# Kernel tuning notes

Measured on AMD Instinct MI355X. Metric: run time of the kernel, lower is better.

The kernel has to match this reference:

```python
import jax, jax.numpy as jnp
import numpy as np

N = 50000      # nodes
E = 800000     # edges
G = 512        # graphs
H = 256        # hidden_dim
T = 32         # tag embedding dim
L = 4          # num_layers
EPS = 1e-5


def setup_inputs() -> dict:
    key = jax.random.key(0)
    ks = jax.random.split(key, 16)
    x = jax.random.randint(ks[0], (N,), 0, 100)
    tags = jax.random.randint(ks[1], (N,), 0, 3)
    edge_index = jax.random.randint(ks[2], (2, E), 0, N)
    batch = jnp.sort(jax.random.randint(ks[3], (N,), 0, G))
    s = 1.0 / np.sqrt(H)
    atom_emb = jax.random.normal(ks[4], (100, H), jnp.float32)
    tag_emb = jax.random.normal(ks[5], (3, T), jnp.float32)
    Wp = jax.random.normal(ks[6], (H + T, H), jnp.float32) * (1.0 / np.sqrt(H + T))
    bp = jnp.zeros((H,), jnp.float32)
    gcn_W = jax.random.normal(ks[7], (L, H, H), jnp.float32) * s
    gcn_b = jnp.zeros((L, H), jnp.float32)
    bn_g = jnp.ones((L, H), jnp.float32)
    bn_b = jnp.zeros((L, H), jnp.float32)
    W1 = jax.random.normal(ks[8], (H, H // 2), jnp.float32) * s
    b1 = jnp.zeros((H // 2,), jnp.float32)
    W2 = jax.random.normal(ks[9], (H // 2, 1), jnp.float32) * (1.0 / np.sqrt(H // 2))
    b2 = jnp.zeros((1,), jnp.float32)
    return dict(x=x, tags=tags, edge_index=edge_index, batch=batch,
                atom_emb=atom_emb, tag_emb=tag_emb, Wp=Wp, bp=bp,
                gcn_W=gcn_W, gcn_b=gcn_b, bn_g=bn_g, bn_b=bn_b,
                W1=W1, b1=b1, W2=W2, b2=b2)


def _gcn_conv(h, W, b, src, dst, dinv):
    # PyG GCNConv: x' = W x, symmetric normalization with self-loops.
    hw = h @ W                                   # [N, H]
    norm = dinv[src] * dinv[dst]                 # [E]
    msg = hw[src] * norm[:, None]                # [E, H]  (gather)
    agg = jax.ops.segment_sum(msg, dst, num_segments=N)  # scatter-add
    agg = agg + hw * (dinv * dinv)[:, None]      # self-loop term
    return agg + b


def _batch_norm(x, g, b):
    mu = jnp.mean(x, axis=0)
    var = jnp.var(x, axis=0)
    return (x - mu) * jax.lax.rsqrt(var + EPS) * g + b


def reference(x, tags, edge_index, batch, atom_emb, tag_emb, Wp, bp,
              gcn_W, gcn_b, bn_g, bn_b, W1, b1, W2, b2):
    src, dst = edge_index[0], edge_index[1]
    # degree with self-loops (gcn_norm counts on the dst/col index)
    deg = jax.ops.segment_sum(jnp.ones((E,), jnp.float32), dst, num_segments=N) + 1.0
    dinv = jax.lax.rsqrt(deg)

    h = jnp.concatenate([atom_emb[x], tag_emb[tags]], axis=1) @ Wp + bp  # [N, H]
    for l in range(L):
        res = h
        h = _gcn_conv(h, gcn_W[l], gcn_b[l], src, dst, dinv)
        h = jax.nn.relu(_batch_norm(h, bn_g[l], bn_b[l]))
        h = h + res                                  # dropout is identity in eval

    # global mean pool over graphs
    sums = jax.ops.segment_sum(h, batch, num_segments=G)
    cnts = jax.ops.segment_sum(jnp.ones((N,), jnp.float32), batch, num_segments=G)
    pooled = sums / jnp.maximum(cnts, 1.0)[:, None]  # [G, H]

    hid = jax.nn.relu(pooled @ W1 + b1)
    energy = hid @ W2 + b2                           # [G, 1]
    return energy.squeeze(-1)
```

## Files before the change

kernel.cpp:

```cpp
#include <hip/hip_runtime.h>
#include <hip/hip_bf16.h>

#define NN 50000
#define EE 800000
#define GG 512
#define HH 256
#define TT 32
#define LL 4
#define EPSF 1e-5f

typedef __attribute__((ext_vector_type(8))) short short8;
typedef __attribute__((ext_vector_type(4))) float float4v;

__device__ inline unsigned short f2b(float f) {
    unsigned u = __float_as_uint(f);
    unsigned r = (u + 0x7FFFu + ((u >> 16) & 1u)) >> 16;
    return (unsigned short)r;
}
__device__ inline float4 bf4_to_f4(ushort4 u) {
    float4 f;
    f.x = __uint_as_float((unsigned)u.x << 16);
    f.y = __uint_as_float((unsigned)u.y << 16);
    f.z = __uint_as_float((unsigned)u.z << 16);
    f.w = __uint_as_float((unsigned)u.w << 16);
    return f;
}

__global__ void k_degree(const int* __restrict__ dst, int* __restrict__ cnt, int E) {
    int e = blockIdx.x * 256 + threadIdx.x;
    if (e < E) atomicAdd(&cnt[dst[e]], 1);
}

__global__ void k_dinv(const int* __restrict__ cnt, float* __restrict__ dinv, int N) {
    int i = blockIdx.x * 256 + threadIdx.x;
    if (i < N) dinv[i] = rsqrtf((float)cnt[i] + 1.0f);
}

__global__ void k_scan1(const int* __restrict__ cnt, int* __restrict__ incl,
                        int* __restrict__ bsum, int N) {
    __shared__ int s[1024];
    int i = blockIdx.x * 1024 + threadIdx.x;
    int v = (i < N) ? cnt[i] : 0;
    s[threadIdx.x] = v;
    __syncthreads();
    for (int off = 1; off < 1024; off <<= 1) {
        int t = (threadIdx.x >= off) ? s[threadIdx.x - off] : 0;
        __syncthreads();
        s[threadIdx.x] += t;
        __syncthreads();
    }
    if (i < N) incl[i] = s[threadIdx.x];
    if (threadIdx.x == 1023) bsum[blockIdx.x] = s[1023];
}

__global__ void k_scan2(int* __restrict__ bsum, int nb) {
    __shared__ int s[64];
    int v = (threadIdx.x < nb) ? bsum[threadIdx.x] : 0;
    s[threadIdx.x] = v;
    __syncthreads();
    for (int off = 1; off < 64; off <<= 1) {
        int t = (threadIdx.x >= off) ? s[threadIdx.x - off] : 0;
        __syncthreads();
        s[threadIdx.x] += t;
        __syncthreads();
    }
    if (threadIdx.x < nb) bsum[threadIdx.x] = s[threadIdx.x] - v;
}

__global__ void k_scan3(int* __restrict__ rs, const int* __restrict__ cnt,
                        const int* __restrict__ boff, int N) {
    int i = blockIdx.x * 256 + threadIdx.x;
    if (i < N) rs[i] = rs[i] + boff[i >> 10] - cnt[i];
}

__global__ void k_scatter(const int* __restrict__ src, const int* __restrict__ dst,
                          const int* __restrict__ rs, int* __restrict__ cur,
                          int* __restrict__ csr, int E) {
    int e = blockIdx.x * 256 + threadIdx.x;
    if (e >= E) return;
    int d = dst[e];
    int p = rs[d] + atomicAdd(&cur[d], 1);
    csr[p] = src[e];
}

__global__ void k_wprep(const float* __restrict__ W, unsigned short* __restrict__ Wt) {
    int l = blockIdx.y;
    int n = blockIdx.x * 4 + (threadIdx.x >> 6);
    int kq = (threadIdx.x & 63) * 4;
    const float* Wl = W + (size_t)l * HH * HH;
    ushort4 o;
    o.x = f2b(Wl[(size_t)(kq + 0) * HH + n]);
    o.y = f2b(Wl[(size_t)(kq + 1) * HH + n]);
    o.z = f2b(Wl[(size_t)(kq + 2) * HH + n]);
    o.w = f2b(Wl[(size_t)(kq + 3) * HH + n]);
    *(ushort4*)(Wt + (size_t)l * HH * HH + (size_t)n * HH + kq) = o;
}

__global__ void k_proj(const float* __restrict__ atom_emb, const float* __restrict__ tag_emb,
                       const float* __restrict__ Wp, const float* __restrict__ bp,
                       float* __restrict__ aref, float* __restrict__ tref) {
    int r = blockIdx.x;
    int j = threadIdx.x;
    if (r < 100) {
        float acc = bp[j];
        for (int k = 0; k < HH; ++k) acc += atom_emb[r * HH + k] * Wp[(size_t)k * HH + j];
        aref[r * HH + j] = acc;
    } else {
        int tr = r - 100;
        float acc = 0.f;
        for (int k = 0; k < TT; ++k) acc += tag_emb[tr * TT + k] * Wp[(size_t)(HH + k) * HH + j];
        tref[tr * HH + j] = acc;
    }
}

__global__ void k_h0(const int* __restrict__ x, const int* __restrict__ tags,
                     const float* __restrict__ aref, const float* __restrict__ tref,
                     unsigned short* __restrict__ hb, int N) {
    int n = blockIdx.x;
    int lane = threadIdx.x;
    float4 a = ((const float4*)(aref + (size_t)x[n] * HH))[lane];
    float4 t = ((const float4*)(tref + (size_t)tags[n] * HH))[lane];
    ushort4 u;
    u.x = f2b(a.x + t.x); u.y = f2b(a.y + t.y);
    u.z = f2b(a.z + t.z); u.w = f2b(a.w + t.w);
    ((ushort4*)(hb + (size_t)n * HH))[lane] = u;
}

__global__ __launch_bounds__(256) void k_gemm(const unsigned short* __restrict__ hb,
                                              const unsigned short* __restrict__ Wt,
                                              const float* __restrict__ dinv,
                                              unsigned short* __restrict__ hwb, int M) {
    __shared__ unsigned short As[128][72];
    __shared__ unsigned short Bs[128][72];
    int t = threadIdx.x;
    int lane = t & 63, w = t >> 6;
    int wr = w >> 1, wc = w & 1;
    int l15 = lane & 15, l4 = lane >> 4;
    int row0 = blockIdx.y * 128, col0 = blockIdx.x * 128;
    float4v acc[4][4];
#pragma unroll
    for (int i = 0; i < 4; ++i)
#pragma unroll
        for (int j = 0; j < 4; ++j) acc[i][j] = (float4v)0.f;

    for (int k0 = 0; k0 < 256; k0 += 64) {
        if (k0) __syncthreads();
#pragma unroll
        for (int u = 0; u < 4; ++u) {
            int idx = u * 256 + t;
            int r = idx >> 3;
            int c = (idx & 7) * 8;
            *(uint4*)&As[r][c] = *(const uint4*)(hb + (size_t)(row0 + r) * 256 + k0 + c);
            *(uint4*)&Bs[r][c] = *(const uint4*)(Wt + (size_t)(col0 + r) * 256 + k0 + c);
        }
        __syncthreads();
#pragma unroll
        for (int kk = 0; kk < 64; kk += 32) {
            short8 a[4], b[4];
#pragma unroll
            for (int i = 0; i < 4; ++i)
                a[i] = *(const short8*)&As[wr * 64 + i * 16 + l15][kk + l4 * 8];
#pragma unroll
            for (int i = 0; i < 4; ++i)
                b[i] = *(const short8*)&Bs[wc * 64 + i * 16 + l15][kk + l4 * 8];
#pragma unroll
            for (int mi = 0; mi < 4; ++mi)
#pragma unroll
                for (int ni = 0; ni < 4; ++ni)
                    acc[mi][ni] = __builtin_amdgcn_mfma_f32_16x16x32_bf16(
                        a[mi], b[ni], acc[mi][ni], 0, 0, 0);
        }
    }
#pragma unroll
    for (int mi = 0; mi < 4; ++mi) {
        int mb = row0 + wr * 64 + mi * 16 + l4 * 4;
        float dv[4];
#pragma unroll
        for (int r = 0; r < 4; ++r) dv[r] = (mb + r < M) ? dinv[mb + r] : 0.f;
#pragma unroll
        for (int ni = 0; ni < 4; ++ni) {
            int n = col0 + wc * 64 + ni * 16 + l15;
#pragma unroll
            for (int r = 0; r < 4; ++r) {
                if (mb + r < M)
                    hwb[(size_t)(mb + r) * 256 + n] = f2b(acc[mi][ni][r] * dv[r]);
            }
        }
    }
}

__global__ void k_agg(const unsigned short* __restrict__ hwb, float* __restrict__ agg,
                      const int* __restrict__ csr, const int* __restrict__ rs,
                      const int* __restrict__ cnt, const float* __restrict__ dinv,
                      const float* __restrict__ bias, int N) {
    int wave = threadIdx.x >> 6;
    int lane = threadIdx.x & 63;
    int n = blockIdx.x * 4 + wave;
    if (n >= N) return;
    float dn = dinv[n];
    int e = rs[n];
    int end = e + cnt[n];
    float4 acc = bf4_to_f4(((const ushort4*)(hwb + (size_t)n * HH))[lane]);
    for (; e + 8 <= end; e += 8) {
        int s0 = csr[e],     s1 = csr[e + 1], s2 = csr[e + 2], s3 = csr[e + 3];
        int s4 = csr[e + 4], s5 = csr[e + 5], s6 = csr[e + 6], s7 = csr[e + 7];
        float4 m0 = bf4_to_f4(((const ushort4*)(hwb + (size_t)s0 * HH))[lane]);
        float4 m1 = bf4_to_f4(((const ushort4*)(hwb + (size_t)s1 * HH))[lane]);
        float4 m2 = bf4_to_f4(((const ushort4*)(hwb + (size_t)s2 * HH))[lane]);
        float4 m3 = bf4_to_f4(((const ushort4*)(hwb + (size_t)s3 * HH))[lane]);
        float4 m4 = bf4_to_f4(((const ushort4*)(hwb + (size_t)s4 * HH))[lane]);
        float4 m5 = bf4_to_f4(((const ushort4*)(hwb + (size_t)s5 * HH))[lane]);
        float4 m6 = bf4_to_f4(((const ushort4*)(hwb + (size_t)s6 * HH))[lane]);
        float4 m7 = bf4_to_f4(((const ushort4*)(hwb + (size_t)s7 * HH))[lane]);
        acc.x += ((m0.x + m1.x) + (m2.x + m3.x)) + ((m4.x + m5.x) + (m6.x + m7.x));
        acc.y += ((m0.y + m1.y) + (m2.y + m3.y)) + ((m4.y + m5.y) + (m6.y + m7.y));
        acc.z += ((m0.z + m1.z) + (m2.z + m3.z)) + ((m4.z + m5.z) + (m6.z + m7.z));
        acc.w += ((m0.w + m1.w) + (m2.w + m3.w)) + ((m4.w + m5.w) + (m6.w + m7.w));
    }
    for (; e + 4 <= end; e += 4) {
        int s0 = csr[e], s1 = csr[e + 1], s2 = csr[e + 2], s3 = csr[e + 3];
        float4 m0 = bf4_to_f4(((const ushort4*)(hwb + (size_t)s0 * HH))[lane]);
        float4 m1 = bf4_to_f4(((const ushort4*)(hwb + (size_t)s1 * HH))[lane]);
        float4 m2 = bf4_to_f4(((const ushort4*)(hwb + (size_t)s2 * HH))[lane]);
        float4 m3 = bf4_to_f4(((const ushort4*)(hwb + (size_t)s3 * HH))[lane]);
        acc.x += (m0.x + m1.x) + (m2.x + m3.x);
        acc.y += (m0.y + m1.y) + (m2.y + m3.y);
        acc.z += (m0.z + m1.z) + (m2.z + m3.z);
        acc.w += (m0.w + m1.w) + (m2.w + m3.w);
    }
    for (; e < end; ++e) {
        int s = csr[e];
        float4 m = bf4_to_f4(((const ushort4*)(hwb + (size_t)s * HH))[lane]);
        acc.x += m.x; acc.y += m.y; acc.z += m.z; acc.w += m.w;
    }
    float4 b = ((const float4*)bias)[lane];
    float4 r;
    r.x = acc.x * dn + b.x; r.y = acc.y * dn + b.y;
    r.z = acc.z * dn + b.z; r.w = acc.w * dn + b.w;
    ((float4*)(agg + (size_t)n * HH))[lane] = r;
}

__global__ __launch_bounds__(256) void k_bnstats(const float4* __restrict__ agg,
                                                 float* __restrict__ colsum,
                                                 float* __restrict__ colsq, int N) {
    __shared__ float4 ssum[4][64];
    __shared__ float4 ssq[4][64];
    int lane = threadIdx.x & 63;
    int wv = threadIdx.x >> 6;
    int rows_per = (N + gridDim.x - 1) / gridDim.x;
    int r0 = blockIdx.x * rows_per;
    int r1 = r0 + rows_per; if (r1 > N) r1 = N;
    float4 s = make_float4(0.f, 0.f, 0.f, 0.f);
    float4 s2 = make_float4(0.f, 0.f, 0.f, 0.f);
    for (int r = r0 + wv; r < r1; r += 4) {
        float4 v = agg[(size_t)r * 64 + lane];
        s.x += v.x; s.y += v.y; s.z += v.z; s.w += v.w;
        s2.x += v.x * v.x; s2.y += v.y * v.y; s2.z += v.z * v.z; s2.w += v.w * v.w;
    }
    ssum[wv][lane] = s;
    ssq[wv][lane] = s2;
    __syncthreads();
    int j = lane * 4;
    if (wv == 0) {
        float4 a = ssum[0][lane], b = ssum[1][lane], c = ssum[2][lane], d = ssum[3][lane];
        atomicAdd(&colsum[j + 0], a.x + b.x + c.x + d.x);
        atomicAdd(&colsum[j + 1], a.y + b.y + c.y + d.y);
        atomicAdd(&colsum[j + 2], a.z + b.z + c.z + d.z);
        atomicAdd(&colsum[j + 3], a.w + b.w + c.w + d.w);
    } else if (wv == 1) {
        float4 a = ssq[0][lane], b = ssq[1][lane], c = ssq[2][lane], d = ssq[3][lane];
        atomicAdd(&colsq[j + 0], a.x + b.x + c.x + d.x);
        atomicAdd(&colsq[j + 1], a.y + b.y + c.y + d.y);
        atomicAdd(&colsq[j + 2], a.z + b.z + c.z + d.z);
        atomicAdd(&colsq[j + 3], a.w + b.w + c.w + d.w);
    }
}

__global__ void k_epi(const float4* __restrict__ agg, ushort4* __restrict__ hb,
                      const float4* __restrict__ colsum, const float4* __restrict__ colsq,
                      const float4* __restrict__ g4, const float4* __restrict__ b4,
                      int total, float invN) {
    int idx = blockIdx.x * 256 + threadIdx.x;
    if (idx >= total) return;
    int q = idx & 63;
    float4 a = agg[idx];
    float4 s = colsum[q], s2 = colsq[q], g = g4[q], b = b4[q];
    float4 hv = bf4_to_f4(hb[idx]);
    float mu, var, v;
    mu = s.x * invN; var = s2.x * invN - mu * mu;
    v = (a.x - mu) * rsqrtf(var + EPSF) * g.x + b.x; hv.x += fmaxf(v, 0.f);
    mu = s.y * invN; var = s2.y * invN - mu * mu;
    v = (a.y - mu) * rsqrtf(var + EPSF) * g.y + b.y; hv.y += fmaxf(v, 0.f);
    mu = s.z * invN; var = s2.z * invN - mu * mu;
    v = (a.z - mu) * rsqrtf(var + EPSF) * g.z + b.z; hv.z += fmaxf(v, 0.f);
    mu = s.w * invN; var = s2.w * invN - mu * mu;
    v = (a.w - mu) * rsqrtf(var + EPSF) * g.w + b.w; hv.w += fmaxf(v, 0.f);
    ushort4 u;
    u.x = f2b(hv.x); u.y = f2b(hv.y); u.z = f2b(hv.z); u.w = f2b(hv.w);
    hb[idx] = u;
}

__global__ void k_ginit(int* __restrict__ gstart, int G, int N) {
    int g = blockIdx.x * 256 + threadIdx.x;
    if (g <= G) gstart[g] = N;
}

__global__ void k_gbound(const int* __restrict__ batch, int* __restrict__ gstart, int N) {
    int n = blockIdx.x * 256 + threadIdx.x;
    if (n >= N) return;
    int b = batch[n];
    int prev = (n == 0) ? -1 : batch[n - 1];
    for (int g = prev + 1; g <= b; ++g) gstart[g] = n;
}

__global__ void k_pool(const unsigned short* __restrict__ hb, const int* __restrict__ gstart,
                       float* __restrict__ pooled) {
    __shared__ float4 sm[4][64];
    int g = blockIdx.x;
    int t = threadIdx.x;
    int lane = t & 63, wv = t >> 6;
    int s = gstart[g], e = gstart[g + 1];
    float4 acc = make_float4(0.f, 0.f, 0.f, 0.f);
    for (int n = s + wv; n < e; n += 4) {
        float4 v = bf4_to_f4(((const ushort4*)(hb + (size_t)n * HH))[lane]);
        acc.x += v.x; acc.y += v.y; acc.z += v.z; acc.w += v.w;
    }
    sm[wv][lane] = acc;
    __syncthreads();
    if (wv == 0) {
        float4 a = sm[0][lane], b = sm[1][lane], c = sm[2][lane], d = sm[3][lane];
        float inv = 1.0f / fmaxf((float)(e - s), 1.0f);
        float4 r;
        r.x = (a.x + b.x + c.x + d.x) * inv;
        r.y = (a.y + b.y + c.y + d.y) * inv;
        r.z = (a.z + b.z + c.z + d.z) * inv;
        r.w = (a.w + b.w + c.w + d.w) * inv;
        ((float4*)pooled)[(size_t)g * 64 + lane] = r;
    }
}

__global__ void k_head(const float* __restrict__ pooled,
                       const float* __restrict__ W1, const float* __restrict__ b1,
                       const float* __restrict__ W2, const float* __restrict__ b2,
                       float* __restrict__ out) {
    __shared__ float prow[256];
    __shared__ float hred[128];
    int g = blockIdx.x, t = threadIdx.x;
    prow[t] = pooled[(size_t)g * HH + t];
    prow[t + 128] = pooled[(size_t)g * HH + t + 128];
    __syncthreads();
    float acc = b1[t];
    for (int k = 0; k < HH; ++k) acc += prow[k] * W1[(size_t)k * 128 + t];
    float hid = fmaxf(acc, 0.f);
    hred[t] = hid * W2[t];
    __syncthreads();
    for (int off = 64; off > 0; off >>= 1) {
        if (t < off) hred[t] += hred[t + off];
        __syncthreads();
    }
    if (t == 0) out[g] = hred[0] + b2[0];
}

extern "C" void kernel_launch(void* const* d_in, const int* in_sizes, int n_in,
                              void* d_out, int out_size, void* d_ws, size_t ws_size,
                              hipStream_t stream) {
    const int* x        = (const int*)d_in[0];
    const int* tags     = (const int*)d_in[1];
    const int* ei       = (const int*)d_in[2];
    const int* batch    = (const int*)d_in[3];
    const float* atom_e = (const float*)d_in[4];
    const float* tag_e  = (const float*)d_in[5];
    const float* Wp     = (const float*)d_in[6];
    const float* bp     = (const float*)d_in[7];
    const float* gcn_W  = (const float*)d_in[8];
    const float* gcn_b  = (const float*)d_in[9];
    const float* bn_g   = (const float*)d_in[10];
    const float* bn_b   = (const float*)d_in[11];
    const float* W1     = (const float*)d_in[12];
    const float* b1     = (const float*)d_in[13];
    const float* W2     = (const float*)d_in[14];
    const float* b2     = (const float*)d_in[15];
    float* out = (float*)d_out;

    const int N = NN, E = EE, G = GG, H = HH;
    const int Mpad = ((N + 127) / 128) * 128;

    char* p = (char*)d_ws;
    auto alloc = [&](size_t bytes) {
        void* r = (void*)p;
        p += (bytes + 255) & ~(size_t)255;
        return r;
    };
    unsigned short* hb  = (unsigned short*)alloc((size_t)Mpad * H * 2);
    unsigned short* hwb = (unsigned short*)alloc((size_t)Mpad * H * 2);
    unsigned short* Wt  = (unsigned short*)alloc((size_t)LL * H * H * 2);
    float* agg  = (float*)alloc((size_t)N * H * 4);
    float* dinv = (float*)alloc((size_t)N * 4);
    int* cnt    = (int*)alloc((size_t)N * 4);
    int* rs     = (int*)alloc((size_t)N * 4);
    int* cur    = (int*)alloc((size_t)N * 4);
    int* csr    = (int*)alloc((size_t)E * 4);
    int* bsum   = (int*)alloc(64 * 4);
    float* aref = (float*)alloc(100 * (size_t)H * 4);
    float* tref = (float*)alloc(3 * (size_t)H * 4);
    float* cstat= (float*)alloc(2 * (size_t)H * 4);
    int* gstart = (int*)alloc((size_t)(G + 1) * 4);
    float* pooled = (float*)alloc((size_t)G * H * 4);

    const int* src = ei;
    const int* dst = ei + E;

    hipMemsetAsync(cnt, 0, (size_t)N * 4, stream);
    hipMemsetAsync(cur, 0, (size_t)N * 4, stream);

    k_degree<<<(E + 255) / 256, 256, 0, stream>>>(dst, cnt, E);
    k_dinv<<<(N + 255) / 256, 256, 0, stream>>>(cnt, dinv, N);

    int nb = (N + 1023) / 1024;
    k_scan1<<<nb, 1024, 0, stream>>>(cnt, rs, bsum, N);
    k_scan2<<<1, 64, 0, stream>>>(bsum, nb);
    k_scan3<<<(N + 255) / 256, 256, 0, stream>>>(rs, cnt, bsum, N);
    k_scatter<<<(E + 255) / 256, 256, 0, stream>>>(src, dst, rs, cur, csr, E);

    k_ginit<<<(G + 256) / 256, 256, 0, stream>>>(gstart, G, N);
    k_gbound<<<(N + 255) / 256, 256, 0, stream>>>(batch, gstart, N);

    k_wprep<<<dim3(64, LL), 256, 0, stream>>>(gcn_W, Wt);
    k_proj<<<103, 256, 0, stream>>>(atom_e, tag_e, Wp, bp, aref, tref);
    k_h0<<<N, 64, 0, stream>>>(x, tags, aref, tref, hb, N);

    for (int l = 0; l < LL; ++l) {
        k_gemm<<<dim3(2, Mpad / 128), 256, 0, stream>>>(
            hb, Wt + (size_t)l * H * H, dinv, hwb, N);
        k_agg<<<(N + 3) / 4, 256, 0, stream>>>(hwb, agg, csr, rs, cnt, dinv,
                                               gcn_b + (size_t)l * H, N);
        hipMemsetAsync(cstat, 0, 2 * (size_t)H * 4, stream);
        k_bnstats<<<512, 256, 0, stream>>>((const float4*)agg, cstat, cstat + H, N);
        k_epi<<<(N * 64 + 255) / 256, 256, 0, stream>>>(
            (const float4*)agg, (ushort4*)hb,
            (const float4*)cstat, (const float4*)(cstat + H),
            (const float4*)(bn_g + (size_t)l * H), (const float4*)(bn_b + (size_t)l * H),
            N * 64, 1.0f / (float)N);
    }

    k_pool<<<G, 256, 0, stream>>>(hb, gstart, pooled);
    k_head<<<G, 128, 0, stream>>>(pooled, W1, b1, W2, b2, out);
}
```

Baseline: 899.9 us.

## Fuse whole GNN pipeline into one cooperative persistent megakernel

Replaces the chain of many small kernel launches (degree, scan, CSR build, projection, per-layer GEMM/aggregate/batchnorm/epilogue, pooling, head) with a single cooperative kernel using grid-wide syncs between phases. The aggregate buffer is stored in bf16 instead of fp32, and the final layer's batchnorm/residual epilogue is folded into the pooling pass. This targets launch overhead and reduces memory traffic, at the cost of grid-sync latency and possibly lower occupancy for the GEMM and gather phases.

```diff
diff --git a/kernel.cpp b/kernel.cpp
--- a/kernel.cpp
+++ b/kernel.cpp
@@ -1,5 +1,8 @@
 #include <hip/hip_runtime.h>
 #include <hip/hip_bf16.h>
+#include <hip/hip_cooperative_groups.h>
+
+namespace cg = cooperative_groups;
 
 #define NN 50000
 #define EE 800000
@@ -8,6 +11,7 @@
 #define TT 32
 #define LL 4
 #define EPSF 1e-5f
+#define MPAD 50048
 
 typedef __attribute__((ext_vector_type(8))) short short8;
 typedef __attribute__((ext_vector_type(4))) float float4v;
@@ -16,6 +20,10 @@
     unsigned u = __float_as_uint(f);
     unsigned r = (u + 0x7FFFu + ((u >> 16) & 1u)) >> 16;
     return (unsigned short)r;
+}
+__device__ inline unsigned pack2(float lo, float hi) {
+    __hip_bfloat162 b2 = __float22bfloat162_rn(float2{lo, hi});
+    return *reinterpret_cast<unsigned*>(&b2);
 }
 __device__ inline float4 bf4_to_f4(ushort4 u) {
     float4 f;
@@ -26,339 +34,388 @@
     return f;
 }
 
-__global__ void k_degree(const int* __restrict__ dst, int* __restrict__ cnt, int E) {
-    int e = blockIdx.x * 256 + threadIdx.x;
-    if (e < E) atomicAdd(&cnt[dst[e]], 1);
-}
-
-__global__ void k_dinv(const int* __restrict__ cnt, float* __restrict__ dinv, int N) {
-    int i = blockIdx.x * 256 + threadIdx.x;
-    if (i < N) dinv[i] = rsqrtf((float)cnt[i] + 1.0f);
-}
-
-__global__ void k_scan1(const int* __restrict__ cnt, int* __restrict__ incl,
-                        int* __restrict__ bsum, int N) {
-    __shared__ int s[1024];
-    int i = blockIdx.x * 1024 + threadIdx.x;
-    int v = (i < N) ? cnt[i] : 0;
-    s[threadIdx.x] = v;
-    __syncthreads();
-    for (int off = 1; off < 1024; off <<= 1) {
-        int t = (threadIdx.x >= off) ? s[threadIdx.x - off] : 0;
+__global__ __launch_bounds__(256, 4) void k_mega(
+    const int* __restrict__ x, const int* __restrict__ tags,
+    const int* __restrict__ ei, const int* __restrict__ batch,
+    const float* __restrict__ atom_e, const float* __restrict__ tag_e,
+    const float* __restrict__ Wp, const float* __restrict__ bp,
+    const float* __restrict__ gcn_W, const float* __restrict__ gcn_b,
+    const float* __restrict__ bn_g, const float* __restrict__ bn_b,
+    const float* __restrict__ W1, const float* __restrict__ b1,
+    const float* __restrict__ W2, const float* __restrict__ b2,
+    float* __restrict__ out,
+    unsigned short* __restrict__ hb, unsigned short* __restrict__ hwb,
+    unsigned short* __restrict__ Wt, unsigned short* __restrict__ aggb,
+    float* __restrict__ dinv, int* __restrict__ rs, int* __restrict__ csr,
+    int* __restrict__ bsum, float* __restrict__ aref, float* __restrict__ tref,
+    int* __restrict__ gstart, float* __restrict__ pooled,
+    int* __restrict__ cnt, int* __restrict__ cur, float* __restrict__ cstat) {
+
+    cg::grid_group gg = cg::this_grid();
+    __shared__ __align__(16) char smem[36864];
+
+    const int* src = ei;
+    const int* dst = ei + EE;
+    const int T = blockIdx.x * 256 + threadIdx.x;
+    const int NT = gridDim.x * 256;
+    const float invN = 1.0f / (float)NN;
+
+    for (int e = T; e < EE; e += NT) atomicAdd(&cnt[dst[e]], 1);
+    gg.sync();
+
+    const int nch = (NN + 255) / 256;
+    {
+        int* si = (int*)smem;
+        for (int ch = blockIdx.x; ch < nch; ch += gridDim.x) {
+            int i = ch * 256 + threadIdx.x;
+            int v = (i < NN) ? cnt[i] : 0;
+            si[threadIdx.x] = v;
+            __syncthreads();
+            for (int off = 1; off < 256; off <<= 1) {
+                int t = (threadIdx.x >= off) ? si[threadIdx.x - off] : 0;
+                __syncthreads();
+                si[threadIdx.x] += t;
+                __syncthreads();
+            }
+            if (i < NN) rs[i] = si[threadIdx.x];
+            if (threadIdx.x == 255) bsum[ch] = si[255];
+            __syncthreads();
+        }
+    }
+    gg.sync();
+
+    if (blockIdx.x == 0) {
+        int* si = (int*)smem;
+        int v = (threadIdx.x < nch) ? bsum[threadIdx.x] : 0;
+        si[threadIdx.x] = v;
         __syncthreads();
-        s[threadIdx.x] += t;
-        __syncthreads();
-    }
-    if (i < N) incl[i] = s[threadIdx.x];
-    if (threadIdx.x == 1023) bsum[blockIdx.x] = s[1023];
-}
-
-__global__ void k_scan2(int* __restrict__ bsum, int nb) {
-    __shared__ int s[64];
-    int v = (threadIdx.x < nb) ? bsum[threadIdx.x] : 0;
-    s[threadIdx.x] = v;
-    __syncthreads();
-    for (int off = 1; off < 64; off <<= 1) {
-        int t = (threadIdx.x >= off) ? s[threadIdx.x - off] : 0;
-        __syncthreads();
-        s[threadIdx.x] += t;
-        __syncthreads();
-    }
-    if (threadIdx.x < nb) bsum[threadIdx.x] = s[threadIdx.x] - v;
-}
-
-__global__ void k_scan3(int* __restrict__ rs, const int* __restrict__ cnt,
-                        const int* __restrict__ boff, int N) {
-    int i = blockIdx.x * 256 + threadIdx.x;
-    if (i < N) rs[i] = rs[i] + boff[i >> 10] - cnt[i];
-}
-
-__global__ void k_scatter(const int* __restrict__ src, const int* __restrict__ dst,
-                          const int* __restrict__ rs, int* __restrict__ cur,
-                          int* __restrict__ csr, int E) {
-    int e = blockIdx.x * 256 + threadIdx.x;
-    if (e >= E) return;
-    int d = dst[e];
-    int p = rs[d] + atomicAdd(&cur[d], 1);
-    csr[p] = src[e];
-}
-
-__global__ void k_wprep(const float* __restrict__ W, unsigned short* __restrict__ Wt) {
-    int l = blockIdx.y;
-    int n = blockIdx.x * 4 + (threadIdx.x >> 6);
-    int kq = (threadIdx.x & 63) * 4;
-    const float* Wl = W + (size_t)l * HH * HH;
-    ushort4 o;
-    o.x = f2b(Wl[(size_t)(kq + 0) * HH + n]);
-    o.y = f2b(Wl[(size_t)(kq + 1) * HH + n]);
-    o.z = f2b(Wl[(size_t)(kq + 2) * HH + n]);
-    o.w = f2b(Wl[(size_t)(kq + 3) * HH + n]);
-    *(ushort4*)(Wt + (size_t)l * HH * HH + (size_t)n * HH + kq) = o;
-}
-
-__global__ void k_proj(const float* __restrict__ atom_emb, const float* __restrict__ tag_emb,
-                       const float* __restrict__ Wp, const float* __restrict__ bp,
-                       float* __restrict__ aref, float* __restrict__ tref) {
-    int r = blockIdx.x;
-    int j = threadIdx.x;
-    if (r < 100) {
-        float acc = bp[j];
-        for (int k = 0; k < HH; ++k) acc += atom_emb[r * HH + k] * Wp[(size_t)k * HH + j];
-        aref[r * HH + j] = acc;
-    } else {
-        int tr = r - 100;
-        float acc = 0.f;
-        for (int k = 0; k < TT; ++k) acc += tag_emb[tr * TT + k] * Wp[(size_t)(HH + k) * HH + j];
-        tref[tr * HH + j] = acc;
-    }
-}
-
-__global__ void k_h0(const int* __restrict__ x, const int* __restrict__ tags,
-                     const float* __restrict__ aref, const float* __restrict__ tref,
-                     unsigned short* __restrict__ hb, int N) {
-    int n = blockIdx.x;
-    int lane = threadIdx.x;
-    float4 a = ((const float4*)(aref + (size_t)x[n] * HH))[lane];
-    float4 t = ((const float4*)(tref + (size_t)tags[n] * HH))[lane];
-    ushort4 u;
-    u.x = f2b(a.x + t.x); u.y = f2b(a.y + t.y);
-    u.z = f2b(a.z + t.z); u.w = f2b(a.w + t.w);
-    ((ushort4*)(hb + (size_t)n * HH))[lane] = u;
-}
-
-__global__ __launch_bounds__(256) void k_gemm(const unsigned short* __restrict__ hb,
-                                              const unsigned short* __restrict__ Wt,
-                                              const float* __restrict__ dinv,
-                                              unsigned short* __restrict__ hwb, int M) {
-    __shared__ unsigned short As[128][72];
-    __shared__ unsigned short Bs[128][72];
-    int t = threadIdx.x;
-    int lane = t & 63, w = t >> 6;
-    int wr = w >> 1, wc = w & 1;
-    int l15 = lane & 15, l4 = lane >> 4;
-    int row0 = blockIdx.y * 128, col0 = blockIdx.x * 128;
-    float4v acc[4][4];
-#pragma unroll
-    for (int i = 0; i < 4; ++i)
-#pragma unroll
-        for (int j = 0; j < 4; ++j) acc[i][j] = (float4v)0.f;
-
-    for (int k0 = 0; k0 < 256; k0 += 64) {
-        if (k0) __syncthreads();
-#pragma unroll
-        for (int u = 0; u < 4; ++u) {
-            int idx = u * 256 + t;
-            int r = idx >> 3;
-            int c = (idx & 7) * 8;
-            *(uint4*)&As[r][c] = *(const uint4*)(hb + (size_t)(row0 + r) * 256 + k0 + c);
-            *(uint4*)&Bs[r][c] = *(const uint4*)(Wt + (size_t)(col0 + r) * 256 + k0 + c);
-        }
-        __syncthreads();
-#pragma unroll
-        for (int kk = 0; kk < 64; kk += 32) {
-            short8 a[4], b[4];
-#pragma unroll
-            for (int i = 0; i < 4; ++i)
-                a[i] = *(const short8*)&As[wr * 64 + i * 16 + l15][kk + l4 * 8];
-#pragma unroll
-            for (int i = 0; i < 4; ++i)
-                b[i] = *(const short8*)&Bs[wc * 64 + i * 16 + l15][kk + l4 * 8];
-#pragma unroll
-            for (int mi = 0; mi < 4; ++mi)
-#pragma unroll
-                for (int ni = 0; ni < 4; ++ni)
-                    acc[mi][ni] = __builtin_amdgcn_mfma_f32_16x16x32_bf16(
-                        a[mi], b[ni], acc[mi][ni], 0, 0, 0);
-        }
-    }
-#pragma unroll
-    for (int mi = 0; mi < 4; ++mi) {
-        int mb = row0 + wr * 64 + mi * 16 + l4 * 4;
-        float dv[4];
-#pragma unroll
-        for (int r = 0; r < 4; ++r) dv[r] = (mb + r < M) ? dinv[mb + r] : 0.f;
-#pragma unroll
-        for (int ni = 0; ni < 4; ++ni) {
-            int n = col0 + wc * 64 + ni * 16 + l15;
-#pragma unroll
-            for (int r = 0; r < 4; ++r) {
-                if (mb + r < M)
-                    hwb[(size_t)(mb + r) * 256 + n] = f2b(acc[mi][ni][r] * dv[r]);
-            }
-        }
-    }
-}
-
-__global__ void k_agg(const unsigned short* __restrict__ hwb, float* __restrict__ agg,
-                      const int* __restrict__ csr, const int* __restrict__ rs,
-                      const int* __restrict__ cnt, const float* __restrict__ dinv,
-                      const float* __restrict__ bias, int N) {
-    int wave = threadIdx.x >> 6;
-    int lane = threadIdx.x & 63;
-    int n = blockIdx.x * 4 + wave;
-    if (n >= N) return;
-    float dn = dinv[n];
-    int e = rs[n];
-    int end = e + cnt[n];
-    float4 acc = bf4_to_f4(((const ushort4*)(hwb + (size_t)n * HH))[lane]);
-    for (; e + 8 <= end; e += 8) {
-        int s0 = csr[e],     s1 = csr[e + 1], s2 = csr[e + 2], s3 = csr[e + 3];
-        int s4 = csr[e + 4], s5 = csr[e + 5], s6 = csr[e + 6], s7 = csr[e + 7];
-        float4 m0 = bf4_to_f4(((const ushort4*)(hwb + (size_t)s0 * HH))[lane]);
-        float4 m1 = bf4_to_f4(((const ushort4*)(hwb + (size_t)s1 * HH))[lane]);
-        float4 m2 = bf4_to_f4(((const ushort4*)(hwb + (size_t)s2 * HH))[lane]);
-        float4 m3 = bf4_to_f4(((const ushort4*)(hwb + (size_t)s3 * HH))[lane]);
-        float4 m4 = bf4_to_f4(((const ushort4*)(hwb + (size_t)s4 * HH))[lane]);
-        float4 m5 = bf4_to_f4(((const ushort4*)(hwb + (size_t)s5 * HH))[lane]);
-        float4 m6 = bf4_to_f4(((const ushort4*)(hwb + (size_t)s6 * HH))[lane]);
-        float4 m7 = bf4_to_f4(((const ushort4*)(hwb + (size_t)s7 * HH))[lane]);
-        acc.x += ((m0.x + m1.x) + (m2.x + m3.x)) + ((m4.x + m5.x) + (m6.x + m7.x));
-        acc.y += ((m0.y + m1.y) + (m2.y + m3.y)) + ((m4.y + m5.y) + (m6.y + m7.y));
-        acc.z += ((m0.z + m1.z) + (m2.z + m3.z)) + ((m4.z + m5.z) + (m6.z + m7.z));
-        acc.w += ((m0.w + m1.w) + (m2.w + m3.w)) + ((m4.w + m5.w) + (m6.w + m7.w));
-    }
-    for (; e + 4 <= end; e += 4) {
-        int s0 = csr[e], s1 = csr[e + 1], s2 = csr[e + 2], s3 = csr[e + 3];
-        float4 m0 = bf4_to_f4(((const ushort4*)(hwb + (size_t)s0 * HH))[lane]);
-        float4 m1 = bf4_to_f4(((const ushort4*)(hwb + (size_t)s1 * HH))[lane]);
-        float4 m2 = bf4_to_f4(((const ushort4*)(hwb + (size_t)s2 * HH))[lane]);
-        float4 m3 = bf4_to_f4(((const ushort4*)(hwb + (size_t)s3 * HH))[lane]);
-        acc.x += (m0.x + m1.x) + (m2.x + m3.x);
-        acc.y += (m0.y + m1.y) + (m2.y + m3.y);
-        acc.z += (m0.z + m1.z) + (m2.z + m3.z);
-        acc.w += (m0.w + m1.w) + (m2.w + m3.w);
-    }
-    for (; e < end; ++e) {
-        int s = csr[e];
-        float4 m = bf4_to_f4(((const ushort4*)(hwb + (size_t)s * HH))[lane]);
-        acc.x += m.x; acc.y += m.y; acc.z += m.z; acc.w += m.w;
-    }
-    float4 b = ((const float4*)bias)[lane];
-    float4 r;
-    r.x = acc.x * dn + b.x; r.y = acc.y * dn + b.y;
-    r.z = acc.z * dn + b.z; r.w = acc.w * dn + b.w;
-    ((float4*)(agg + (size_t)n * HH))[lane] = r;
-}
-
-__global__ __launch_bounds__(256) void k_bnstats(const float4* __restrict__ agg,
-                                                 float* __restrict__ colsum,
-                                                 float* __restrict__ colsq, int N) {
-    __shared__ float4 ssum[4][64];
-    __shared__ float4 ssq[4][64];
-    int lane = threadIdx.x & 63;
-    int wv = threadIdx.x >> 6;
-    int rows_per = (N + gridDim.x - 1) / gridDim.x;
-    int r0 = blockIdx.x * rows_per;
-    int r1 = r0 + rows_per; if (r1 > N) r1 = N;
-    float4 s = make_float4(0.f, 0.f, 0.f, 0.f);
-    float4 s2 = make_float4(0.f, 0.f, 0.f, 0.f);
-    for (int r = r0 + wv; r < r1; r += 4) {
-        float4 v = agg[(size_t)r * 64 + lane];
-        s.x += v.x; s.y += v.y; s.z += v.z; s.w += v.w;
-        s2.x += v.x * v.x; s2.y += v.y * v.y; s2.z += v.z * v.z; s2.w += v.w * v.w;
-    }
-    ssum[wv][lane] = s;
-    ssq[wv][lane] = s2;
-    __syncthreads();
-    int j = lane * 4;
-    if (wv == 0) {
-        float4 a = ssum[0][lane], b = ssum[1][lane], c = ssum[2][lane], d = ssum[3][lane];
-        atomicAdd(&colsum[j + 0], a.x + b.x + c.x + d.x);
-        atomicAdd(&colsum[j + 1], a.y + b.y + c.y + d.y);
-        atomicAdd(&colsum[j + 2], a.z + b.z + c.z + d.z);
-        atomicAdd(&colsum[j + 3], a.w + b.w + c.w + d.w);
-    } else if (wv == 1) {
-        float4 a = ssq[0][lane], b = ssq[1][lane], c = ssq[2][lane], d = ssq[3][lane];
-        atomicAdd(&colsq[j + 0], a.x + b.x + c.x + d.x);
-        atomicAdd(&colsq[j + 1], a.y + b.y + c.y + d.y);
-        atomicAdd(&colsq[j + 2], a.z + b.z + c.z + d.z);
-        atomicAdd(&colsq[j + 3], a.w + b.w + c.w + d.w);
-    }
-}
-
-__global__ void k_epi(const float4* __restrict__ agg, ushort4* __restrict__ hb,
-                      const float4* __restrict__ colsum, const float4* __restrict__ colsq,
-                      const float4* __restrict__ g4, const float4* __restrict__ b4,
-                      int total, float invN) {
-    int idx = blockIdx.x * 256 + threadIdx.x;
-    if (idx >= total) return;
-    int q = idx & 63;
-    float4 a = agg[idx];
-    float4 s = colsum[q], s2 = colsq[q], g = g4[q], b = b4[q];
-    float4 hv = bf4_to_f4(hb[idx]);
-    float mu, var, v;
-    mu = s.x * invN; var = s2.x * invN - mu * mu;
-    v = (a.x - mu) * rsqrtf(var + EPSF) * g.x + b.x; hv.x += fmaxf(v, 0.f);
-    mu = s.y * invN; var = s2.y * invN - mu * mu;
-    v = (a.y - mu) * rsqrtf(var + EPSF) * g.y + b.y; hv.y += fmaxf(v, 0.f);
-    mu = s.z * invN; var = s2.z * invN - mu * mu;
-    v = (a.z - mu) * rsqrtf(var + EPSF) * g.z + b.z; hv.z += fmaxf(v, 0.f);
-    mu = s.w * invN; var = s2.w * invN - mu * mu;
-    v = (a.w - mu) * rsqrtf(var + EPSF) * g.w + b.w; hv.w += fmaxf(v, 0.f);
-    ushort4 u;
-    u.x = f2b(hv.x); u.y = f2b(hv.y); u.z = f2b(hv.z); u.w = f2b(hv.w);
-    hb[idx] = u;
-}
-
-__global__ void k_ginit(int* __restrict__ gstart, int G, int N) {
-    int g = blockIdx.x * 256 + threadIdx.x;
-    if (g <= G) gstart[g] = N;
-}
-
-__global__ void k_gbound(const int* __restrict__ batch, int* __restrict__ gstart, int N) {
-    int n = blockIdx.x * 256 + threadIdx.x;
-    if (n >= N) return;
-    int b = batch[n];
-    int prev = (n == 0) ? -1 : batch[n - 1];
-    for (int g = prev + 1; g <= b; ++g) gstart[g] = n;
-}
-
-__global__ void k_pool(const unsigned short* __restrict__ hb, const int* __restrict__ gstart,
-                       float* __restrict__ pooled) {
-    __shared__ float4 sm[4][64];
-    int g = blockIdx.x;
-    int t = threadIdx.x;
-    int lane = t & 63, wv = t >> 6;
-    int s = gstart[g], e = gstart[g + 1];
-    float4 acc = make_float4(0.f, 0.f, 0.f, 0.f);
-    for (int n = s + wv; n < e; n += 4) {
-        float4 v = bf4_to_f4(((const ushort4*)(hb + (size_t)n * HH))[lane]);
-        acc.x += v.x; acc.y += v.y; acc.z += v.z; acc.w += v.w;
-    }
-    sm[wv][lane] = acc;
-    __syncthreads();
-    if (wv == 0) {
-        float4 a = sm[0][lane], b = sm[1][lane], c = sm[2][lane], d = sm[3][lane];
-        float inv = 1.0f / fmaxf((float)(e - s), 1.0f);
-        float4 r;
-        r.x = (a.x + b.x + c.x + d.x) * inv;
-        r.y = (a.y + b.y + c.y + d.y) * inv;
-        r.z = (a.z + b.z + c.z + d.z) * inv;
-        r.w = (a.w + b.w + c.w + d.w) * inv;
-        ((float4*)pooled)[(size_t)g * 64 + lane] = r;
-    }
-}
-
-__global__ void k_head(const float* __restrict__ pooled,
-                       const float* __restrict__ W1, const float* __restrict__ b1,
-                       const float* __restrict__ W2, const float* __restrict__ b2,
-                       float* __restrict__ out) {
-    __shared__ float prow[256];
-    __shared__ float hred[128];
-    int g = blockIdx.x, t = threadIdx.x;
-    prow[t] = pooled[(size_t)g * HH + t];
-    prow[t + 128] = pooled[(size_t)g * HH + t + 128];
-    __syncthreads();
-    float acc = b1[t];
-    for (int k = 0; k < HH; ++k) acc += prow[k] * W1[(size_t)k * 128 + t];
-    float hid = fmaxf(acc, 0.f);
-    hred[t] = hid * W2[t];
-    __syncthreads();
-    for (int off = 64; off > 0; off >>= 1) {
-        if (t < off) hred[t] += hred[t + off];
-        __syncthreads();
-    }
-    if (t == 0) out[g] = hred[0] + b2[0];
+        for (int off = 1; off < 256; off <<= 1) {
+            int t = (threadIdx.x >= off) ? si[threadIdx.x - off] : 0;
+            __syncthreads();
+            si[threadIdx.x] += t;
+            __syncthreads();
+        }
+        if (threadIdx.x < nch) bsum[threadIdx.x] = si[threadIdx.x] - v;
+    }
+    gg.sync();
+
+    for (int i = T; i < NN; i += NT) {
+        int c = cnt[i];
+        rs[i] = rs[i] + bsum[i >> 8] - c;
+        dinv[i] = rsqrtf((float)c + 1.0f);
+    }
+    gg.sync();
+
+    for (int e = T; e < EE; e += NT) {
+        int d = dst[e];
+        int p = rs[d] + atomicAdd(&cur[d], 1);
+        csr[p] = src[e];
+    }
+    for (int n = T; n < NN; n += NT) {
+        int b = batch[n];
+        int prev = (n == 0) ? -1 : batch[n - 1];
+        for (int g = prev + 1; g <= b; ++g) gstart[g] = n;
+        if (n == NN - 1)
+            for (int g = b + 1; g <= GG; ++g) gstart[g] = NN;
+    }
+    for (int it = T; it < LL * 256 * 64; it += NT) {
+        int l = it >> 14;
+        int rem = it & 16383;
+        int n = rem >> 6;
+        int kq = (rem & 63) * 4;
+        const float* Wl = gcn_W + (size_t)l * HH * HH;
+        ushort4 o;
+        o.x = f2b(Wl[(size_t)(kq + 0) * HH + n]);
+        o.y = f2b(Wl[(size_t)(kq + 1) * HH + n]);
+        o.z = f2b(Wl[(size_t)(kq + 2) * HH + n]);
+        o.w = f2b(Wl[(size_t)(kq + 3) * HH + n]);
+        *(ushort4*)(Wt + (size_t)l * HH * HH + (size_t)n * HH + kq) = o;
+    }
+    for (int it = T; it < 103 * 256; it += NT) {
+        int r = it >> 8;
+        int j = it & 255;
+        if (r < 100) {
+            float acc = bp[j];
+            for (int k = 0; k < HH; ++k) acc += atom_e[r * HH + k] * Wp[(size_t)k * HH + j];
+            aref[r * HH + j] = acc;
+        } else {
+            int tr = r - 100;
+            float acc = 0.f;
+            for (int k = 0; k < TT; ++k) acc += tag_e[tr * TT + k] * Wp[(size_t)(HH + k) * HH + j];
+            tref[tr * HH + j] = acc;
+        }
+    }
+    gg.sync();
+
+    for (int i = T; i < NN * 64; i += NT) {
+        int n = i >> 6, lane = i & 63;
+        float4 a = ((const float4*)(aref + (size_t)x[n] * HH))[lane];
+        float4 t4 = ((const float4*)(tref + (size_t)tags[n] * HH))[lane];
+        unsigned lo = pack2(a.x + t4.x, a.y + t4.y);
+        unsigned hi = pack2(a.z + t4.z, a.w + t4.w);
+        ((uint2*)hb)[i] = make_uint2(lo, hi);
+    }
+    gg.sync();
+
+    for (int l = 0; l < LL; ++l) {
+        if (l > 0) {
+            float* sc = (float*)smem;
+            float* sh = sc + 256;
+            {
+                int t = threadIdx.x;
+                const float* cs = cstat + (size_t)(l - 1) * 512;
+                float mu = cs[t] * invN;
+                float var = cs[256 + t] * invN - mu * mu;
+                float s = bn_g[(size_t)(l - 1) * HH + t] * rsqrtf(var + EPSF);
+                sc[t] = s;
+                sh[t] = bn_b[(size_t)(l - 1) * HH + t] - mu * s;
+            }
+            __syncthreads();
+            for (int i = T; i < NN * 64; i += NT) {
+                int q = (i & 63) * 4;
+                float4 a = bf4_to_f4(((const ushort4*)aggb)[i]);
+                float4 hv = bf4_to_f4(((const ushort4*)hb)[i]);
+                hv.x += fmaxf(a.x * sc[q + 0] + sh[q + 0], 0.f);
+                hv.y += fmaxf(a.y * sc[q + 1] + sh[q + 1], 0.f);
+                hv.z += fmaxf(a.z * sc[q + 2] + sh[q + 2], 0.f);
+                hv.w += fmaxf(a.w * sc[q + 3] + sh[q + 3], 0.f);
+                unsigned lo = pack2(hv.x, hv.y);
+                unsigned hi = pack2(hv.z, hv.w);
+                ((uint2*)hb)[i] = make_uint2(lo, hi);
+            }
+            gg.sync();
+        }
+
+        {
+            unsigned short (*As)[72] = (unsigned short(*)[72])smem;
+            unsigned short (*Bs)[72] = (unsigned short(*)[72])(smem + 18432);
+            const unsigned short* Wl = Wt + (size_t)l * HH * HH;
+            int t = threadIdx.x;
+            int lane = t & 63, w = t >> 6;
+            int wr = w >> 1, wc = w & 1;
+            int l15 = lane & 15, l4 = lane >> 4;
+            int ntile = (MPAD / 128) * 2;
+            for (int job = blockIdx.x; job < ntile; job += gridDim.x) {
+                int row0 = (job >> 1) * 128, col0 = (job & 1) * 128;
+                float4v acc[4][4];
+#pragma unroll
+                for (int i = 0; i < 4; ++i)
+#pragma unroll
+                    for (int j = 0; j < 4; ++j) acc[i][j] = (float4v)0.f;
+                for (int k0 = 0; k0 < 256; k0 += 64) {
+                    __syncthreads();
+#pragma unroll
+                    for (int u = 0; u < 4; ++u) {
+                        int idx = u * 256 + t;
+                        int r = idx >> 3;
+                        int c = (idx & 7) * 8;
+                        int grow = row0 + r;
+                        uint4 av = make_uint4(0u, 0u, 0u, 0u);
+                        if (grow < NN) av = *(const uint4*)(hb + (size_t)grow * 256 + k0 + c);
+                        *(uint4*)&As[r][c] = av;
+                        *(uint4*)&Bs[r][c] = *(const uint4*)(Wl + (size_t)(col0 + r) * 256 + k0 + c);
+                    }
+                    __syncthreads();
+#pragma unroll
+                    for (int kk = 0; kk < 64; kk += 32) {
+                        short8 a[4], b[4];
+#pragma unroll
+                        for (int i = 0; i < 4; ++i)
+                            a[i] = *(const short8*)&As[wr * 64 + i * 16 + l15][kk + l4 * 8];
+#pragma unroll
+                        for (int i = 0; i < 4; ++i)
+                            b[i] = *(const short8*)&Bs[wc * 64 + i * 16 + l15][kk + l4 * 8];
+#pragma unroll
+                        for (int mi = 0; mi < 4; ++mi)
+#pragma unroll
+                            for (int ni = 0; ni < 4; ++ni)
+                                acc[mi][ni] = __builtin_amdgcn_mfma_f32_16x16x32_bf16(
+                                    a[mi], b[ni], acc[mi][ni], 0, 0, 0);
+                    }
+                }
+#pragma unroll
+                for (int mi = 0; mi < 4; ++mi) {
+                    int mb = row0 + wr * 64 + mi * 16 + l4 * 4;
+                    float dv[4];
+#pragma unroll
+                    for (int r = 0; r < 4; ++r) dv[r] = (mb + r < NN) ? dinv[mb + r] : 0.f;
+#pragma unroll
+                    for (int ni = 0; ni < 4; ++ni) {
+                        int n = col0 + wc * 64 + ni * 16 + l15;
+#pragma unroll
+                        for (int r = 0; r < 4; ++r) {
+                            if (mb + r < NN)
+                                hwb[(size_t)(mb + r) * 256 + n] = f2b(acc[mi][ni][r] * dv[r]);
+                        }
+                    }
+                }
+                __syncthreads();
+            }
+        }
+        gg.sync();
+
+        {
+            const float* bias = gcn_b + (size_t)l * HH;
+            int wave = threadIdx.x >> 6;
+            int lane = threadIdx.x & 63;
+            for (int base = blockIdx.x * 4; base < NN; base += gridDim.x * 4) {
+                int n = base + wave;
+                if (n >= NN) continue;
+                float dn = dinv[n];
+                int e = rs[n];
+                int end = e + cnt[n];
+                float4 acc = bf4_to_f4(((const ushort4*)(hwb + (size_t)n * HH))[lane]);
+                for (; e + 8 <= end; e += 8) {
+                    int s0 = csr[e],     s1 = csr[e + 1], s2 = csr[e + 2], s3 = csr[e + 3];
+                    int s4 = csr[e + 4], s5 = csr[e + 5], s6 = csr[e + 6], s7 = csr[e + 7];
+                    float4 m0 = bf4_to_f4(((const ushort4*)(hwb + (size_t)s0 * HH))[lane]);
+                    float4 m1 = bf4_to_f4(((const ushort4*)(hwb + (size_t)s1 * HH))[lane]);
+                    float4 m2 = bf4_to_f4(((const ushort4*)(hwb + (size_t)s2 * HH))[lane]);
+                    float4 m3 = bf4_to_f4(((const ushort4*)(hwb + (size_t)s3 * HH))[lane]);
+                    float4 m4 = bf4_to_f4(((const ushort4*)(hwb + (size_t)s4 * HH))[lane]);
+                    float4 m5 = bf4_to_f4(((const ushort4*)(hwb + (size_t)s5 * HH))[lane]);
+                    float4 m6 = bf4_to_f4(((const ushort4*)(hwb + (size_t)s6 * HH))[lane]);
+                    float4 m7 = bf4_to_f4(((const ushort4*)(hwb + (size_t)s7 * HH))[lane]);
+                    acc.x += ((m0.x + m1.x) + (m2.x + m3.x)) + ((m4.x + m5.x) + (m6.x + m7.x));
+                    acc.y += ((m0.y + m1.y) + (m2.y + m3.y)) + ((m4.y + m5.y) + (m6.y + m7.y));
+                    acc.z += ((m0.z + m1.z) + (m2.z + m3.z)) + ((m4.z + m5.z) + (m6.z + m7.z));
+                    acc.w += ((m0.w + m1.w) + (m2.w + m3.w)) + ((m4.w + m5.w) + (m6.w + m7.w));
+                }
+                for (; e + 4 <= end; e += 4) {
+                    int s0 = csr[e], s1 = csr[e + 1], s2 = csr[e + 2], s3 = csr[e + 3];
+                    float4 m0 = bf4_to_f4(((const ushort4*)(hwb + (size_t)s0 * HH))[lane]);
+                    float4 m1 = bf4_to_f4(((const ushort4*)(hwb + (size_t)s1 * HH))[lane]);
+                    float4 m2 = bf4_to_f4(((const ushort4*)(hwb + (size_t)s2 * HH))[lane]);
+                    float4 m3 = bf4_to_f4(((const ushort4*)(hwb + (size_t)s3 * HH))[lane]);
+                    acc.x += (m0.x + m1.x) + (m2.x + m3.x);
+                    acc.y += (m0.y + m1.y) + (m2.y + m3.y);
+                    acc.z += (m0.z + m1.z) + (m2.z + m3.z);
+                    acc.w += (m0.w + m1.w) + (m2.w + m3.w);
+                }
+                for (; e < end; ++e) {
+                    int s = csr[e];
+                    float4 m = bf4_to_f4(((const ushort4*)(hwb + (size_t)s * HH))[lane]);
+                    acc.x += m.x; acc.y += m.y; acc.z += m.z; acc.w += m.w;
+                }
+                float4 b = ((const float4*)bias)[lane];
+                ushort4 u;
+                u.x = f2b(acc.x * dn + b.x); u.y = f2b(acc.y * dn + b.y);
+                u.z = f2b(acc.z * dn + b.z); u.w = f2b(acc.w * dn + b.w);
+                ((ushort4*)(aggb + (size_t)n * HH))[lane] = u;
+            }
+        }
+        gg.sync();
+
+        {
+            float* colsum = cstat + (size_t)l * 512;
+            float* colsq = colsum + 256;
+            float4 (*ssum)[64] = (float4(*)[64])smem;
+            float4 (*ssq)[64] = (float4(*)[64])(smem + 4096);
+            int lane = threadIdx.x & 63;
+            int wv = threadIdx.x >> 6;
+            int rows_per = (NN + gridDim.x - 1) / gridDim.x;
+            int r0 = blockIdx.x * rows_per;
+            int r1 = r0 + rows_per; if (r1 > NN) r1 = NN;
+            float4 s = make_float4(0.f, 0.f, 0.f, 0.f);
+            float4 s2 = make_float4(0.f, 0.f, 0.f, 0.f);
+            for (int r = r0 + wv; r < r1; r += 4) {
+                float4 v = bf4_to_f4(((const ushort4*)aggb)[(size_t)r * 64 + lane]);
+                s.x += v.x; s.y += v.y; s.z += v.z; s.w += v.w;
+                s2.x += v.x * v.x; s2.y += v.y * v.y; s2.z += v.z * v.z; s2.w += v.w * v.w;
+            }
+            ssum[wv][lane] = s;
+            ssq[wv][lane] = s2;
+            __syncthreads();
+            int j = lane * 4;
+            if (wv == 0) {
+                float4 a = ssum[0][lane], b = ssum[1][lane], c = ssum[2][lane], d = ssum[3][lane];
+                atomicAdd(&colsum[j + 0], a.x + b.x + c.x + d.x);
+                atomicAdd(&colsum[j + 1], a.y + b.y + c.y + d.y);
+                atomicAdd(&colsum[j + 2], a.z + b.z + c.z + d.z);
+                atomicAdd(&colsum[j + 3], a.w + b.w + c.w + d.w);
+            } else if (wv == 1) {
+                float4 a = ssq[0][lane], b = ssq[1][lane], c = ssq[2][lane], d = ssq[3][lane];
+                atomicAdd(&colsq[j + 0], a.x + b.x + c.x + d.x);
+                atomicAdd(&colsq[j + 1], a.y + b.y + c.y + d.y);
+                atomicAdd(&colsq[j + 2], a.z + b.z + c.z + d.z);
+                atomicAdd(&colsq[j + 3], a.w + b.w + c.w + d.w);
+            }
+            __syncthreads();
+        }
+        gg.sync();
+    }
+
+    {
+        const float* colsum = cstat + 3 * 512;
+        const float* colsq = colsum + 256;
+        const float* bng = bn_g + 3 * HH;
+        const float* bnb = bn_b + 3 * HH;
+        float4 (*sm)[64] = (float4(*)[64])smem;
+        int t = threadIdx.x;
+        int lane = t & 63, wv = t >> 6;
+        int col = lane * 4;
+        float4 cs = *(const float4*)(colsum + col);
+        float4 cq = *(const float4*)(colsq + col);
+        float4 g4 = *(const float4*)(bng + col);
+        float4 b4 = *(const float4*)(bnb + col);
+        float4 scl, shf;
+        float mu, var;
+        mu = cs.x * invN; var = cq.x * invN - mu * mu; scl.x = g4.x * rsqrtf(var + EPSF); shf.x = b4.x - mu * scl.x;
+        mu = cs.y * invN; var = cq.y * invN - mu * mu; scl.y = g4.y * rsqrtf(var + EPSF); shf.y = b4.y - mu * scl.y;
+        mu = cs.z * invN; var = cq.z * invN - mu * mu; scl.z = g4.z * rsqrtf(var + EPSF); shf.z = b4.z - mu * scl.z;
+        mu = cs.w * invN; var = cq.w * invN - mu * mu; scl.w = g4.w * rsqrtf(var + EPSF); shf.w = b4.w - mu * scl.w;
+        for (int g = blockIdx.x; g < GG; g += gridDim.x) {
+            int s = gstart[g], e = gstart[g + 1];
+            float4 acc = make_float4(0.f, 0.f, 0.f, 0.f);
+            for (int n = s + wv; n < e; n += 4) {
+                float4 hv = bf4_to_f4(((const ushort4*)hb)[(size_t)n * 64 + lane]);
+                float4 av = bf4_to_f4(((const ushort4*)aggb)[(size_t)n * 64 + lane]);
+                acc.x += hv.x + fmaxf(av.x * scl.x + shf.x, 0.f);
+                acc.y += hv.y + fmaxf(av.y * scl.y + shf.y, 0.f);
+                acc.z += hv.z + fmaxf(av.z * scl.z + shf.z, 0.f);
+                acc.w += hv.w + fmaxf(av.w * scl.w + shf.w, 0.f);
+            }
+            sm[wv][lane] = acc;
+            __syncthreads();
+            if (wv == 0) {
+                float4 a = sm[0][lane], b = sm[1][lane], c = sm[2][lane], d = sm[3][lane];
+                float inv = 1.0f / fmaxf((float)(e - s), 1.0f);
+                float4 r;
+                r.x = (a.x + b.x + c.x + d.x) * inv;
+                r.y = (a.y + b.y + c.y + d.y) * inv;
+                r.z = (a.z + b.z + c.z + d.z) * inv;
+                r.w = (a.w + b.w + c.w + d.w) * inv;
+                ((float4*)pooled)[(size_t)g * 64 + lane] = r;
+            }
+            __syncthreads();
+        }
+    }
+    gg.sync();
+
+    {
+        float* prow = (float*)smem;
+        float* hred = prow + 256;
+        int t = threadIdx.x;
+        for (int g = blockIdx.x; g < GG; g += gridDim.x) {
+            if (t < 128) {
+                prow[t] = pooled[(size_t)g * HH + t];
+                prow[t + 128] = pooled[(size_t)g * HH + t + 128];
+            }
+            __syncthreads();
+            if (t < 128) {
+                float acc = b1[t];
+                for (int k = 0; k < HH; ++k) acc += prow[k] * W1[(size_t)k * 128 + t];
+                hred[t] = fmaxf(acc, 0.f) * W2[t];
+            }
+            __syncthreads();
+            for (int off = 64; off > 0; off >>= 1) {
+                if (t < off) hred[t] += hred[t + off];
+                __syncthreads();
+            }
+            if (t == 0) out[g] = hred[0] + b2[0];
+            __syncthreads();
+        }
+    }
 }
 
 extern "C" void kernel_launch(void* const* d_in, const int* in_sizes, int n_in,
@@ -382,67 +439,48 @@
     const float* b2     = (const float*)d_in[15];
     float* out = (float*)d_out;
 
-    const int N = NN, E = EE, G = GG, H = HH;
-    const int Mpad = ((N + 127) / 128) * 128;
-
     char* p = (char*)d_ws;
     auto alloc = [&](size_t bytes) {
         void* r = (void*)p;
         p += (bytes + 255) & ~(size_t)255;
         return r;
     };
-    unsigned short* hb  = (unsigned short*)alloc((size_t)Mpad * H * 2);
-    unsigned short* hwb = (unsigned short*)alloc((size_t)Mpad * H * 2);
-    unsigned short* Wt  = (unsigned short*)alloc((size_t)LL * H * H * 2);
-    float* agg  = (float*)alloc((size_t)N * H * 4);
-    float* dinv = (float*)alloc((size_t)N * 4);
-    int* cnt    = (int*)alloc((size_t)N * 4);
-    int* rs     = (int*)alloc((size_t)N * 4);
-    int* cur    = (int*)alloc((size_t)N * 4);
-    int* csr    = (int*)alloc((size_t)E * 4);
-    int* bsum   = (int*)alloc(64 * 4);
-    float* aref = (float*)alloc(100 * (size_t)H * 4);
-    float* tref = (float*)alloc(3 * (size_t)H * 4);
-    float* cstat= (float*)alloc(2 * (size_t)H * 4);
-    int* gstart = (int*)alloc((size_t)(G + 1) * 4);
-    float* pooled = (float*)alloc((size_t)G * H * 4);
-
-    const int* src = ei;
-    const int* dst = ei + E;
-
-    hipMemsetAsync(cnt, 0, (size_t)N * 4, stream);
-    hipMemsetAsync(cur, 0, (size_t)N * 4, stream);
-
-    k_degree<<<(E + 255) / 256, 256, 0, stream>>>(dst, cnt, E);
-    k_dinv<<<(N + 255) / 256, 256, 0, stream>>>(cnt, dinv, N);
-
-    int nb = (N + 1023) / 1024;
-    k_scan1<<<nb, 1024, 0, stream>>>(cnt, rs, bsum, N);
-    k_scan2<<<1, 64, 0, stream>>>(bsum, nb);
-    k_scan3<<<(N + 255) / 256, 256, 0, stream>>>(rs, cnt, bsum, N);
-    k_scatter<<<(E + 255) / 256, 256, 0, stream>>>(src, dst, rs, cur, csr, E);
-
-    k_ginit<<<(G + 256) / 256, 256, 0, stream>>>(gstart, G, N);
-    k_gbound<<<(N + 255) / 256, 256, 0, stream>>>(batch, gstart, N);
-
-    k_wprep<<<dim3(64, LL), 256, 0, stream>>>(gcn_W, Wt);
-    k_proj<<<103, 256, 0, stream>>>(atom_e, tag_e, Wp, bp, aref, tref);
-    k_h0<<<N, 64, 0, stream>>>(x, tags, aref, tref, hb, N);
-
-    for (int l = 0; l < LL; ++l) {
-        k_gemm<<<dim3(2, Mpad / 128), 256, 0, stream>>>(
-            hb, Wt + (size_t)l * H * H, dinv, hwb, N);
-        k_agg<<<(N + 3) / 4, 256, 0, stream>>>(hwb, agg, csr, rs, cnt, dinv,
-                                               gcn_b + (size_t)l * H, N);
-        hipMemsetAsync(cstat, 0, 2 * (size_t)H * 4, stream);
-        k_bnstats<<<512, 256, 0, stream>>>((const float4*)agg, cstat, cstat + H, N);
-        k_epi<<<(N * 64 + 255) / 256, 256, 0, stream>>>(
-            (const float4*)agg, (ushort4*)hb,
-            (const float4*)cstat, (const float4*)(cstat + H),
-            (const float4*)(bn_g + (size_t)l * H), (const float4*)(bn_b + (size_t)l * H),
-            N * 64, 1.0f / (float)N);
-    }
-
-    k_pool<<<G, 256, 0, stream>>>(hb, gstart, pooled);
-    k_head<<<G, 128, 0, stream>>>(pooled, W1, b1, W2, b2, out);
+    unsigned short* hb  = (unsigned short*)alloc((size_t)MPAD * HH * 2);
+    unsigned short* hwb = (unsigned short*)alloc((size_t)MPAD * HH * 2);
+    unsigned short* Wt  = (unsigned short*)alloc((size_t)LL * HH * HH * 2);
+    unsigned short* aggb= (unsigned short*)alloc((size_t)NN * HH * 2);
+    float* dinv = (float*)alloc((size_t)NN * 4);
+    int* rs     = (int*)alloc((size_t)NN * 4);
+    int* csr    = (int*)alloc((size_t)EE * 4);
+    int* bsum   = (int*)alloc(256 * 4);
+    float* aref = (float*)alloc(100 * (size_t)HH * 4);
+    float* tref = (float*)alloc(3 * (size_t)HH * 4);
+    int* gstart = (int*)alloc((size_t)(GG + 1) * 4);
+    float* pooled = (float*)alloc((size_t)GG * HH * 4);
+    int* cnt    = (int*)alloc((size_t)NN * 4);
+    int* cur    = (int*)alloc((size_t)NN * 4);
+    float* cstat= (float*)alloc((size_t)LL * 512 * 4);
+    size_t zspan = (size_t)((char*)cstat + (size_t)LL * 512 * 4 - (char*)cnt);
+
+    hipMemsetAsync(cnt, 0, zspan, stream);
+
+    int occ = 0;
+    hipOccupancyMaxActiveBlocksPerMultiprocessor(&occ, (const void*)k_mega, 256, 0);
+    if (occ < 1) occ = 1;
+    if (occ > 4) occ = 4;
+    int grid = occ * 256;
+
+    void* params[] = {
+        (void*)&x, (void*)&tags, (void*)&ei, (void*)&batch,
+        (void*)&atom_e, (void*)&tag_e, (void*)&Wp, (void*)&bp,
+        (void*)&gcn_W, (void*)&gcn_b, (void*)&bn_g, (void*)&bn_b,
+        (void*)&W1, (void*)&b1, (void*)&W2, (void*)&b2,
+        (void*)&out,
+        (void*)&hb, (void*)&hwb, (void*)&Wt, (void*)&aggb,
+        (void*)&dinv, (void*)&rs, (void*)&csr, (void*)&bsum,
+        (void*)&aref, (void*)&tref, (void*)&gstart, (void*)&pooled,
+        (void*)&cnt, (void*)&cur, (void*)&cstat
+    };
+    hipLaunchCooperativeKernel((const void*)k_mega, dim3(grid), dim3(256),
+                               params, 0, stream);
 }
```

Result: slower. 2.145 ms (+138.4%).
